# Optimization experiments

Hardware: AMD Instinct MI355X
Metric: run time of the kernel (lower is better)

## Reference

```python
import jax, jax.numpy as jnp
import numpy as np

CHUNK = 32


def l2norm(x):
    return x * jax.lax.rsqrt(jnp.sum(x * x, -1, keepdims=True) + 1e-6)


def causal_dwconv(x, w):
    # x: (b, l, C), w: (C, 1, k) -- depthwise causal 1D conv (left pad k-1)
    k = w.shape[-1]
    xt = jnp.transpose(x, (0, 2, 1))
    xt = jnp.pad(xt, ((0, 0), (0, 0), (k - 1, 0)))
    y = jax.lax.conv_general_dilated(xt, w, (1,), 'VALID',
                                     dimension_numbers=('NCH', 'OIH', 'NCH'),
                                     feature_group_count=xt.shape[1])
    return jnp.transpose(y, (0, 2, 1))


def delta_rule_chunkwise(q, k, v, beta):
    # q,k: (b,h,L,dk), v: (b,h,L,dv), beta: (b,h,L). L must be divisible by CHUNK.
    b, h, L, dk = q.shape
    dv = v.shape[-1]
    n = L // CHUNK
    q = l2norm(q)
    k = l2norm(k)
    v = v * beta[..., None]
    kb = k * beta[..., None]
    resh = lambda t: t.reshape(b, h, n, CHUNK, t.shape[-1])
    q, k, v, kb = (resh(t) for t in (q, k, v, kb))
    strict = jnp.tril(jnp.ones((CHUNK, CHUNK), bool), -1)
    A = jnp.where(strict, -(kb @ jnp.swapaxes(k, -1, -2)), 0.0)
    eye = jnp.eye(CHUNK, dtype=A.dtype)
    # UT transform: the sequential forward-substitution loop computes T = (I - A)^{-1}
    T = jax.scipy.linalg.solve_triangular(eye - A, jnp.broadcast_to(eye, A.shape), lower=True)
    u = T @ v
    w = T @ kb
    incl = jnp.tril(jnp.ones((CHUNK, CHUNK), bool))  # lower incl. diag

    def step(S, xs):
        q_i, k_i, u_i, w_i = xs
        attn = jnp.where(incl, q_i @ jnp.swapaxes(k_i, -1, -2), 0.0)
        u_hat = u_i - w_i @ S
        o_i = q_i @ S + attn @ u_hat
        return S + jnp.swapaxes(k_i, -1, -2) @ u_hat, o_i

    xs = tuple(jnp.moveaxis(t, 2, 0) for t in (q, k, u, w))
    S0 = jnp.zeros((b, h, dk, dv), q.dtype)
    S, o = jax.lax.scan(step, S0, xs)
    o = jnp.moveaxis(o, 0, 2).reshape(b, h, L, dv)
    return o, S


def branch_stats(x):
    # per-head stats over the feature dim: mean, std(ddof=1), mean|x|, L2 norm
    m = jnp.mean(x, -1, keepdims=True)
    s = jnp.std(x, -1, keepdims=True, ddof=1)
    a = jnp.mean(jnp.abs(x), -1, keepdims=True)
    l = jnp.sqrt(jnp.sum(x * x, -1, keepdims=True))
    return jnp.concatenate([m, s, a, l], -1)


def reference(hidden_states, q_w, k_w, v_w, b_w, qc_w, kc_w, vc_w,
              fir_w1, fir_w3, fir_w7, fir_w31,
              mlp_w1, mlp_b1, mlp_w2, mlp_b2, gate_log_temp, onorm_w, o_w):
    B, L, D = hidden_states.shape
    H = gate_log_temp.shape[0]
    dk = q_w.shape[1] // H
    dv = v_w.shape[1] // H
    # projections + causal short conv + silu
    q = jax.nn.silu(causal_dwconv(hidden_states @ q_w, qc_w))
    k = jax.nn.silu(causal_dwconv(hidden_states @ k_w, kc_w))
    v = jax.nn.silu(causal_dwconv(hidden_states @ v_w, vc_w))
    q = q.reshape(B, L, H, dk)
    k = k.reshape(B, L, H, dk)
    v_direct = v.reshape(B, L, H, dv)
    beta = jax.nn.sigmoid(hidden_states @ b_w)  # (B,L,H)
    delta_out, _ = delta_rule_chunkwise(
        jnp.transpose(q, (0, 2, 1, 3)), jnp.transpose(k, (0, 2, 1, 3)),
        jnp.transpose(v_direct, (0, 2, 1, 3)), jnp.transpose(beta, (0, 2, 1)))
    delta_out = jnp.transpose(delta_out, (0, 2, 1, 3))  # (B,L,H,dv)
    # multi-scale depthwise FIR branches on v
    v_flat = v_direct.reshape(B, L, H * dv)
    firs = [causal_dwconv(v_flat, w).reshape(B, L, H, dv)
            for w in (fir_w1, fir_w3, fir_w7, fir_w31)]
    branches = firs + [delta_out, v_direct]  # num_streams = 6
    S = len(branches)
    stats = jnp.concatenate([branch_stats(x) for x in branches], -1)  # (B,L,H,S*4)
    gate_in = jnp.concatenate([hidden_states, stats.reshape(B, L, H * S * 4)], -1)
    hgate = jax.nn.gelu(gate_in @ mlp_w1 + mlp_b1, approximate=False)
    logits = (hgate @ mlp_w2 + mlp_b2).reshape(B, L, H, S)
    temp = jax.nn.softplus(gate_log_temp) + 0.5  # min_gate_temp = 0.5
    weights = jax.nn.softmax(logits / temp[None, None, :, None], axis=-1)
    fused = sum(weights[..., i, None] * br for i, br in enumerate(branches))
    # RMSNorm over head_v_dim (eps=1e-5)
    fused = fused * jax.lax.rsqrt(jnp.mean(fused * fused, -1, keepdims=True) + 1e-5) * onorm_w
    return fused.reshape(B, L, H * dv) @ o_w


def setup_inputs() -> dict:
    key = jax.random.key(0)
    B, L, D, H = 2, 2048, 1024, 4
    dk = dv = D // H
    S = 6
    ks = iter(jax.random.split(key, 32))
    nrm = lambda shape, s=0.02: jax.random.normal(next(ks), shape, jnp.float32) * s

    def fir(kw):
        # delta init (last tap = 1) plus small noise
        base = jnp.zeros((H * dv, 1, kw), jnp.float32).at[:, 0, -1].set(1.0)
        return base + nrm((H * dv, 1, kw))

    gate_in_dim = D + S * 4 * H  # 1120
    hgd = D * 2 // 2             # 1024
    b2 = np.zeros(H * S, np.float32)
    for h in range(H):
        b2[h * S + S - 1] = 2.0  # value_bias_init on direct-value stream
    return {
        'hidden_states': jax.random.normal(next(ks), (B, L, D), jnp.float32),
        'q_w': nrm((D, D)), 'k_w': nrm((D, D)), 'v_w': nrm((D, D)),
        'b_w': nrm((D, H)),
        'qc_w': nrm((D, 1, 4), 0.3), 'kc_w': nrm((D, 1, 4), 0.3), 'vc_w': nrm((D, 1, 4), 0.3),
        'fir_w1': fir(1), 'fir_w3': fir(3), 'fir_w7': fir(7), 'fir_w31': fir(31),
        'mlp_w1': nrm((gate_in_dim, hgd)), 'mlp_b1': jnp.zeros((hgd,), jnp.float32),
        'mlp_w2': nrm((hgd, H * S)), 'mlp_b2': jnp.asarray(b2),
        'gate_log_temp': jnp.zeros((H,), jnp.float32),
        'onorm_w': jnp.ones((dv,), jnp.float32),
        'o_w': nrm((D, D)),
    }
```

## Files before the change

### kernel.cpp

```cpp
#include <hip/hip_runtime.h>
#include <hip/hip_bf16.h>
#include <math.h>

#define B_ 2
#define L_ 2048
#define D_ 1024
#define H_ 4
#define NC 64

typedef unsigned short ushort_t;
typedef __bf16 bf16x8 __attribute__((ext_vector_type(8)));
typedef float f32x4 __attribute__((ext_vector_type(4)));
typedef ushort_t u16x8 __attribute__((ext_vector_type(8)));
typedef short s16x8 __attribute__((ext_vector_type(8)));
typedef short s16x4 __attribute__((ext_vector_type(4)));

__device__ __forceinline__ ushort_t f2bs(float f) {
    __hip_bfloat16 h = __float2bfloat16(f);
    ushort_t u;
    __builtin_memcpy(&u, &h, 2);
    return u;
}

__device__ __forceinline__ float wred(float v) {
    v += __shfl_down(v, 32);
    v += __shfl_down(v, 16);
    v += __shfl_down(v, 8);
    v += __shfl_down(v, 4);
    v += __shfl_down(v, 2);
    v += __shfl_down(v, 1);
    return v;
}

__device__ __forceinline__ void gload16(const void* g, void* l) {
    __builtin_amdgcn_global_load_lds((const __attribute__((address_space(1))) void*)g,
                                     (__attribute__((address_space(3))) void*)l, 16, 0, 0);
}

__device__ __forceinline__ s16x4 pack4(float a, float b, float c, float d) {
    ushort4 u;
    u.x = f2bs(a); u.y = f2bs(b); u.z = f2bs(c); u.w = f2bs(d);
    return __builtin_bit_cast(s16x4, u);
}
__device__ __forceinline__ bf16x8 cat8(s16x4 lo, s16x4 hi) {
    s16x8 r = __builtin_shufflevector(lo, hi, 0, 1, 2, 3, 4, 5, 6, 7);
    return __builtin_bit_cast(bf16x8, r);
}

__global__ __launch_bounds__(256) void tcast_k(const float* __restrict__ W,
                                               ushort_t* __restrict__ WT, int K, int N) {
    __shared__ float tile[32 * 33];
    const int k0 = blockIdx.y << 5, n0 = blockIdx.x << 5;
    for (int e = threadIdx.x; e < 1024; e += 256)
        tile[(e >> 5) * 33 + (e & 31)] = W[(size_t)(k0 + (e >> 5)) * N + n0 + (e & 31)];
    __syncthreads();
    for (int e = threadIdx.x; e < 1024; e += 256)
        WT[(size_t)(n0 + (e >> 5)) * K + k0 + (e & 31)] = f2bs(tile[(e & 31) * 33 + (e >> 5)]);
}

__global__ __launch_bounds__(256) void cast_k(const float* __restrict__ x,
                                              ushort_t* __restrict__ y) {
    const int i = blockIdx.x * 256 + threadIdx.x;
    const float4 v = *(const float4*)&x[(size_t)i * 4];
    ushort4 p;
    p.x = f2bs(v.x); p.y = f2bs(v.y); p.z = f2bs(v.z); p.w = f2bs(v.w);
    *(ushort4*)&y[(size_t)i * 4] = p;
}

template <int ACT>
__global__ __launch_bounds__(256) void gemm_bf(const ushort_t* __restrict__ A,
                                               const ushort_t* __restrict__ Bt,
                                               const float* __restrict__ bias,
                                               float* __restrict__ C,
                                               int M, int N, int K) {
    __shared__ ushort_t As[128 * 32];
    __shared__ ushort_t Bs[128 * 32];
    const int t = threadIdx.x;
    const int wv = t >> 6, l = t & 63;
    const int m0 = blockIdx.y << 7, n0 = blockIdx.x << 7;
    const int wm = wv & 1, wn = wv >> 1;
    const int q4 = l >> 4, c16 = l & 15;
    f32x4 acc[4][4];
#pragma unroll
    for (int i = 0; i < 4; ++i)
#pragma unroll
        for (int j = 0; j < 4; ++j) {
            f32x4 z = {0.f, 0.f, 0.f, 0.f};
            acc[i][j] = z;
        }
    const int srow = (l >> 2);
    const int scol = (l & 3) << 3;
    for (int k0 = 0; k0 < K; k0 += 32) {
        __syncthreads();
#pragma unroll
        for (int si = 0; si < 2; ++si) {
            const int s = wv * 2 + si;
            gload16(&A[(size_t)(m0 + s * 16 + srow) * K + k0 + scol], &As[s * 512]);
            gload16(&Bt[(size_t)(n0 + s * 16 + srow) * K + k0 + scol], &Bs[s * 512]);
        }
        __syncthreads();
        bf16x8 af[4], bff[4];
#pragma unroll
        for (int mi = 0; mi < 4; ++mi)
            af[mi] = *(const bf16x8*)&As[(wm * 64 + mi * 16 + c16) * 32 + q4 * 8];
#pragma unroll
        for (int ni = 0; ni < 4; ++ni)
            bff[ni] = *(const bf16x8*)&Bs[(wn * 64 + ni * 16 + c16) * 32 + q4 * 8];
#pragma unroll
        for (int mi = 0; mi < 4; ++mi)
#pragma unroll
            for (int ni = 0; ni < 4; ++ni)
                acc[mi][ni] = __builtin_amdgcn_mfma_f32_16x16x32_bf16(af[mi], bff[ni],
                                                                     acc[mi][ni], 0, 0, 0);
    }
#pragma unroll
    for (int mi = 0; mi < 4; ++mi)
#pragma unroll
        for (int ni = 0; ni < 4; ++ni)
#pragma unroll
            for (int r = 0; r < 4; ++r) {
                const int row = m0 + wm * 64 + mi * 16 + q4 * 4 + r;
                const int col = n0 + wn * 64 + ni * 16 + c16;
                float v = acc[mi][ni][r];
                if (ACT == 1) {
                    v += bias[col];
                    v = 0.5f * v * (1.0f + erff(v * 0.70710678118654752f));
                }
                C[(size_t)row * N + col] = v;
            }
}

template <int DO_NORM, int EMIT_F32, int EMIT_BF>
__global__ __launch_bounds__(256) void convql_k(const float* __restrict__ X,
                                                const float* __restrict__ cw,
                                                float* __restrict__ Y,
                                                ushort_t* __restrict__ Ybf) {
    __shared__ float xs[35 * 256];
    const int bid = blockIdx.x;
    const int h = bid & 3, lt = (bid >> 2) & 63, b = bid >> 8;
    const int t = threadIdx.x;
    const int l0 = lt << 5;
    const int cg = (h << 8) | t;
    for (int e = t; e < 35 * 256; e += 256) {
        const int r = e >> 8, c = e & 255;
        const int gl = l0 + r - 3;
        xs[e] = (gl >= 0) ? X[((size_t)(b * L_) + gl) * 3072 + (h << 8) + c] : 0.f;
    }
    const float w0 = cw[cg * 4 + 0], w1 = cw[cg * 4 + 1];
    const float w2 = cw[cg * 4 + 2], w3 = cw[cg * 4 + 3];
    __syncthreads();
    float yr[32];
#pragma unroll
    for (int l = 0; l < 32; ++l) {
        const float a = xs[(l + 0) * 256 + t] * w0 + xs[(l + 1) * 256 + t] * w1 +
                        xs[(l + 2) * 256 + t] * w2 + xs[(l + 3) * 256 + t] * w3;
        yr[l] = a / (1.f + expf(-a));
    }
    if (DO_NORM) {
        __syncthreads();
#pragma unroll
        for (int l = 0; l < 32; ++l) xs[l * 256 + t] = yr[l];
        __syncthreads();
        const int wv = t >> 6, lane = t & 63;
#pragma unroll
        for (int ri = 0; ri < 8; ++ri) {
            const int r = wv * 8 + ri;
            float4 v = *(float4*)&xs[r * 256 + lane * 4];
            float ss = v.x * v.x + v.y * v.y + v.z * v.z + v.w * v.w;
            ss = wred(ss);
            ss = __shfl(ss, 0);
            const float s = rsqrtf(ss + 1e-6f);
            v.x *= s; v.y *= s; v.z *= s; v.w *= s;
            const size_t go = ((size_t)(b * L_) + l0 + r) * 1024 + (h << 8) + lane * 4;
            if (EMIT_F32) *(float4*)&Y[go] = v;
            if (EMIT_BF) {
                ushort4 p;
                p.x = f2bs(v.x); p.y = f2bs(v.y); p.z = f2bs(v.z); p.w = f2bs(v.w);
                *(ushort4*)&Ybf[go] = p;
            }
        }
    } else {
#pragma unroll
        for (int l = 0; l < 32; ++l)
            if (EMIT_F32) Y[((size_t)(b * L_) + l0 + l) * 1024 + cg] = yr[l];
    }
}

__global__ __launch_bounds__(256) void fir_k(const float* __restrict__ V,
                                             const float* __restrict__ w1w,
                                             const float* __restrict__ w3w,
                                             const float* __restrict__ w7w,
                                             const float* __restrict__ w31w,
                                             float* __restrict__ o1,
                                             float* __restrict__ o3,
                                             float* __restrict__ o7,
                                             float* __restrict__ o31) {
    __shared__ float xs[62 * 256];
    const int bid = blockIdx.x;
    const int h = bid & 3, lt = (bid >> 2) & 63, b = bid >> 8;
    const int t = threadIdx.x;
    const int l0 = lt << 5;
    const int cg = (h << 8) | t;
    for (int e = t; e < 62 * 256; e += 256) {
        const int r = e >> 8, c = e & 255;
        const int gl = l0 + r - 30;
        xs[e] = (gl >= 0) ? V[((size_t)(b * L_) + gl) * 1024 + (h << 8) + c] : 0.f;
    }
    float lw31[31], lw7[7], lw3[3];
#pragma unroll
    for (int j = 0; j < 31; ++j) lw31[j] = w31w[cg * 31 + j];
#pragma unroll
    for (int j = 0; j < 7; ++j) lw7[j] = w7w[cg * 7 + j];
#pragma unroll
    for (int j = 0; j < 3; ++j) lw3[j] = w3w[cg * 3 + j];
    const float lw1 = w1w[cg];
    __syncthreads();
    for (int l = 0; l < 32; ++l) {
        float a31 = 0.f, a7 = 0.f, a3 = 0.f, v = 0.f;
#pragma unroll
        for (int j = 0; j < 31; ++j) {
            v = xs[(l + j) * 256 + t];
            a31 += v * lw31[j];
            if (j >= 24) a7 += v * lw7[j - 24];
            if (j >= 28) a3 += v * lw3[j - 28];
        }
        const size_t go = ((size_t)(b * L_) + l0 + l) * 1024 + cg;
        o31[go] = a31;
        o7[go] = a7;
        o3[go] = a3;
        o1[go] = v * lw1;
    }
}

__global__ __launch_bounds__(64) void beta_k(const float* __restrict__ hs,
                                             const float* __restrict__ bw,
                                             float* __restrict__ beta,
                                             ushort_t* __restrict__ gin) {
    const int row = blockIdx.x;
    const int lane = threadIdx.x;
    float a0 = 0, a1 = 0, a2 = 0, a3 = 0;
    const float* hp = hs + (size_t)row * D_;
    ushort_t* gp = gin + (size_t)row * 1120;
    for (int c = lane; c < D_; c += 64) {
        const float x = hp[c];
        gp[c] = f2bs(x);
        a0 += x * bw[c * 4 + 0];
        a1 += x * bw[c * 4 + 1];
        a2 += x * bw[c * 4 + 2];
        a3 += x * bw[c * 4 + 3];
    }
    a0 = wred(a0); a1 = wred(a1); a2 = wred(a2); a3 = wred(a3);
    if (lane == 0) {
        float* o = beta + (size_t)row * 4;
        o[0] = 1.f / (1.f + expf(-a0));
        o[1] = 1.f / (1.f + expf(-a1));
        o[2] = 1.f / (1.f + expf(-a2));
        o[3] = 1.f / (1.f + expf(-a3));
    }
}

__global__ __launch_bounds__(256) void prep2_k(const ushort_t* __restrict__ qbf,
                                               const ushort_t* __restrict__ kbf,
                                               const float* __restrict__ vg,
                                               const float* __restrict__ beta,
                                               ushort_t* __restrict__ qfr,
                                               ushort_t* __restrict__ wfr,
                                               float* __restrict__ ufr,
                                               ushort_t* __restrict__ atfr,
                                               ushort_t* __restrict__ ktfr) {
    __shared__ ushort_t k_lds[32 * 264];
    __shared__ ushort_t kT_lds[256 * 32];
    __shared__ ushort_t vT_lds[256 * 32];
    __shared__ float Am[32 * 33];
    __shared__ float Tm[32 * 33];
    __shared__ ushort_t Tb[32 * 40];
    __shared__ ushort_t at_s[32 * 40];
    __shared__ float beta_s[32];
    const int bid = blockIdx.x;
    const int bh = bid >> 6, ci = bid & 63;
    const int b = bh >> 2, h = bh & 3;
    const int t = threadIdx.x;
    const int wv = t >> 6, lane = t & 63;
    const int mi = wv & 1, ni = wv >> 1;
    const int l16 = lane & 15, quad = lane >> 4;
    const size_t cb = (size_t)bid;
    const size_t grow = ((size_t)(b * L_ + ci * 32)) * 1024 + (h << 8);
    const f32x4 z4 = {0.f, 0.f, 0.f, 0.f};

    if (t < 32) beta_s[t] = beta[(size_t)(b * L_ + ci * 32 + t) * 4 + h];
#pragma unroll
    for (int j = 0; j < 4; ++j) {
        const int idx = j * 2048 + t * 8, r = idx >> 8, c = idx & 255;
        *(u16x8*)&k_lds[r * 264 + c] = *(const u16x8*)&kbf[grow + (size_t)r * 1024 + c];
    }
#pragma unroll
    for (int j = 0; j < 8; ++j) {
        const int e = j * 1024 + t * 4, r = e >> 8, c = e & 255;
        const float4 v4 = *(const float4*)&vg[grow + (size_t)r * 1024 + c];
        const float vv[4] = {v4.x, v4.y, v4.z, v4.w};
#pragma unroll
        for (int x = 0; x < 4; ++x) {
            const int cc = c + x;
            const int sp = (r >> 3) ^ ((cc >> 1) & 3);
            vT_lds[cc * 32 + sp * 8 + (r & 7)] = f2bs(vv[x]);
        }
    }
    f32x4 g = z4, atv = z4;
#pragma unroll
    for (int s = 0; s < 8; ++s) {
        const bf16x8 a =
            *(const bf16x8*)&kbf[grow + (size_t)(mi * 16 + l16) * 1024 + s * 32 + (quad << 3)];
        const bf16x8 bb =
            *(const bf16x8*)&kbf[grow + (size_t)(ni * 16 + l16) * 1024 + s * 32 + (quad << 3)];
        const bf16x8 qa =
            *(const bf16x8*)&qbf[grow + (size_t)(mi * 16 + l16) * 1024 + s * 32 + (quad << 3)];
        g = __builtin_amdgcn_mfma_f32_16x16x32_bf16(a, bb, g, 0, 0, 0);
        atv = __builtin_amdgcn_mfma_f32_16x16x32_bf16(qa, bb, atv, 0, 0, 0);
        if (ni == 0) {
            const size_t ga = grow + (size_t)(mi * 16 + l16) * 1024 + s * 32 + (quad << 2);
            const ushort4 q0 = *(const ushort4*)&qbf[ga];
            const ushort4 q1 = *(const ushort4*)&qbf[ga + 16];
            ushort_t* qd = &qfr[((cb * 2 + mi) * 8 + s) * 512 + lane * 8];
            *(ushort4*)qd = q0;
            *(ushort4*)(qd + 4) = q1;
        }
    }
    __syncthreads();
#pragma unroll
    for (int r = 0; r < 4; ++r) {
        const int row = mi * 16 + (quad << 2) + r;
        const int col = ni * 16 + l16;
        Am[row * 33 + col] = (col < row) ? -beta_s[row] * g[r] : 0.f;
        Tm[row * 33 + col] = (row == col) ? 1.f : 0.f;
        at_s[row * 40 + col] = (col <= row) ? f2bs(atv[r]) : (ushort_t)0;
    }
#pragma unroll
    for (int j = 0; j < 8; ++j) {
        const int e = j * 1024 + t * 4, r = e >> 8, c = e & 255;
#pragma unroll
        for (int x = 0; x < 4; ++x) {
            const int cc = c + x;
            const int sp = (r >> 3) ^ ((cc >> 1) & 3);
            kT_lds[cc * 32 + sp * 8 + (r & 7)] = k_lds[r * 264 + cc];
        }
    }
    __syncthreads();
    if (wv < 2) {
        const int ra = (wv * 16 + l16) * 40 + (quad << 2);
        const ushort4 a0 = *(const ushort4*)&at_s[ra];
        const ushort4 a1 = *(const ushort4*)&at_s[ra + 16];
        ushort_t* ad = &atfr[(cb * 2 + wv) * 512 + lane * 8];
        *(ushort4*)ad = a0;
        *(ushort4*)(ad + 4) = a1;
    }
#pragma unroll
    for (int j2 = 0; j2 < 4; ++j2) {
        const int tc = wv * 4 + j2;
        const int d = tc * 16 + l16;
        const int x = (d >> 1) & 3;
        const int base = d * 32 + ((quad & 1) << 2);
        const ushort4 k0 = *(const ushort4*)&kT_lds[base + ((((quad >> 1) + 0) ^ x) << 3)];
        const ushort4 k1 = *(const ushort4*)&kT_lds[base + ((((quad >> 1) + 2) ^ x) << 3)];
        ushort_t* kd = &ktfr[(cb * 16 + tc) * 512 + lane * 8];
        *(ushort4*)kd = k0;
        *(ushort4*)(kd + 4) = k1;
    }
    for (int i = 1; i < 32; ++i) {
        if (t < 32) {
            float s = 0.f;
            for (int j = 0; j < i; ++j) s += Am[i * 33 + j] * Tm[j * 33 + t];
            Tm[i * 33 + t] += s;
        }
        __syncthreads();
    }
#pragma unroll
    for (int j = 0; j < 4; ++j) {
        const int e = j * 256 + t, i = e >> 5, jj = e & 31;
        Tb[i * 40 + jj] = f2bs(Tm[i * 33 + jj] * beta_s[jj]);
    }
    __syncthreads();
    const bf16x8 tf = *(const bf16x8*)&Tb[(mi * 16 + l16) * 40 + (quad << 3)];
#pragma unroll
    for (int j = 0; j < 8; ++j) {
        const int nt = ni * 8 + j;
        const int d = (nt << 4) + l16;
        const int sp = quad ^ ((d >> 1) & 3);
        const bf16x8 kb = *(const bf16x8*)&kT_lds[d * 32 + (sp << 3)];
        const bf16x8 vb = *(const bf16x8*)&vT_lds[d * 32 + (sp << 3)];
        const f32x4 wacc = __builtin_amdgcn_mfma_f32_16x16x32_bf16(tf, kb, z4, 0, 0, 0);
        const f32x4 uacc = __builtin_amdgcn_mfma_f32_16x16x32_bf16(tf, vb, z4, 0, 0, 0);
        *(float4*)&ufr[((cb * 16 + nt) * 2 + mi) * 256 + lane * 4] =
            make_float4(uacc[0], uacc[1], uacc[2], uacc[3]);
#pragma unroll
        for (int r = 0; r < 4; ++r) {
            const int row = mi * 16 + (quad << 2) + r;
            k_lds[row * 264 + d] = f2bs(wacc[r]);
        }
    }
    __syncthreads();
    if (wv < 2) {
#pragma unroll
        for (int sp = 0; sp < 8; ++sp) {
            const int rb = (wv * 16 + l16) * 264 + sp * 32 + (quad << 2);
            const ushort4 w0 = *(const ushort4*)&k_lds[rb];
            const ushort4 w1 = *(const ushort4*)&k_lds[rb + 16];
            ushort_t* wd = &wfr[((cb * 2 + wv) * 8 + sp) * 512 + lane * 8];
            *(ushort4*)wd = w0;
            *(ushort4*)(wd + 4) = w1;
        }
    }
}

__global__ __launch_bounds__(64, 1) void scan9_k(const ushort_t* __restrict__ qfr,
                                                 const ushort_t* __restrict__ wfr,
                                                 const float* __restrict__ ufr,
                                                 const ushort_t* __restrict__ atfr,
                                                 const ushort_t* __restrict__ ktfr,
                                                 float* __restrict__ dlt) {
    __shared__ ushort_t qstg[2][16 * 512];
    __shared__ ushort_t wstg[2][16 * 512];
    __shared__ ushort_t atstg[2][2 * 512];
    __shared__ float ustg[2][2 * 256];
    const int l = threadIdx.x;
    const int qd = l >> 4, c = l & 15;
    const int bh = blockIdx.x & 7, tile = blockIdx.x >> 3;
    const int b = bh >> 2, h = bh & 3;

    f32x4 Sacc[16];
    s16x4 SB[16];
#pragma unroll
    for (int tc = 0; tc < 16; ++tc) {
        f32x4 z = {0.f, 0.f, 0.f, 0.f};
        Sacc[tc] = z;
        s16x4 zs = {0, 0, 0, 0};
        SB[tc] = zs;
    }
    s16x8 ktA[16], ktB[16];

    auto stage = [&](int ci, int p) {
        const size_t cb = (size_t)(bh * NC + ci);
        const ushort_t* qsrc = qfr + cb * (16 * 512);
        const ushort_t* wsrc = wfr + cb * (16 * 512);
#pragma unroll
        for (int f = 0; f < 16; ++f) gload16(&qsrc[f * 512 + l * 8], &qstg[p][f * 512]);
#pragma unroll
        for (int f = 0; f < 16; ++f) gload16(&wsrc[f * 512 + l * 8], &wstg[p][f * 512]);
#pragma unroll
        for (int hf = 0; hf < 2; ++hf)
            gload16(&atfr[(cb * 2 + hf) * 512 + l * 8], &atstg[p][hf * 512]);
#pragma unroll
        for (int hf = 0; hf < 2; ++hf)
            gload16(&ufr[((cb * 16 + tile) * 2 + hf) * 256 + l * 4], &ustg[p][hf * 256]);
    };

    {
        const ushort_t* ksrc = ktfr + (size_t)(bh * NC) * (16 * 512);
#pragma unroll
        for (int tc = 0; tc < 16; ++tc) ktA[tc] = *(const s16x8*)&ksrc[tc * 512 + l * 8];
    }
    stage(0, 0);
    asm volatile("s_waitcnt vmcnt(0)" ::: "memory");
    __builtin_amdgcn_sched_barrier(0);

#define SC_BODY(CI, P, KT, KTN)                                                              \
    {                                                                                        \
        asm volatile("s_waitcnt vmcnt(8)" ::: "memory");                                     \
        __builtin_amdgcn_sched_barrier(0);                                                   \
        if ((CI) + 1 < NC) {                                                                 \
            const ushort_t* ksrc = ktfr + (size_t)(bh * NC + (CI) + 1) * (16 * 512);         \
            _Pragma("unroll") for (int tc = 0; tc < 16; ++tc)                                \
                KTN[tc] = *(const s16x8*)&ksrc[tc * 512 + l * 8];                            \
            stage((CI) + 1, (P) ^ 1);                                                        \
        }                                                                                    \
        f32x4 aw[2], oq[2];                                                                  \
        _Pragma("unroll") for (int hf = 0; hf < 2; ++hf) {                                   \
            f32x4 z = {0.f, 0.f, 0.f, 0.f};                                                  \
            aw[hf] = z;                                                                      \
            oq[hf] = z;                                                                      \
        }                                                                                    \
        _Pragma("unroll") for (int sp = 0; sp < 8; ++sp) {                                   \
            const bf16x8 Sop = cat8(SB[2 * sp + 0], SB[2 * sp + 1]);                         \
            _Pragma("unroll") for (int hf = 0; hf < 2; ++hf) {                               \
                const bf16x8 wv8 = *(const bf16x8*)&wstg[P][(hf * 8 + sp) * 512 + l * 8];    \
                const bf16x8 qv8 = *(const bf16x8*)&qstg[P][(hf * 8 + sp) * 512 + l * 8];    \
                aw[hf] = __builtin_amdgcn_mfma_f32_16x16x32_bf16(wv8, Sop, aw[hf], 0, 0, 0); \
                oq[hf] = __builtin_amdgcn_mfma_f32_16x16x32_bf16(qv8, Sop, oq[hf], 0, 0, 0); \
            }                                                                                \
        }                                                                                    \
        s16x4 uhB[2];                                                                        \
        _Pragma("unroll") for (int hf = 0; hf < 2; ++hf) {                                   \
            const float4 uv = *(const float4*)&ustg[P][hf * 256 + l * 4];                    \
            uhB[hf] = pack4(uv.x - aw[hf][0], uv.y - aw[hf][1],                              \
                            uv.z - aw[hf][2], uv.w - aw[hf][3]);                             \
        }                                                                                    \
        const bf16x8 Uop = cat8(uhB[0], uhB[1]);                                             \
        _Pragma("unroll") for (int tc = 0; tc < 16; ++tc) {                                  \
            Sacc[tc] = __builtin_amdgcn_mfma_f32_16x16x32_bf16(                              \
                __builtin_bit_cast(bf16x8, KT[tc]), Uop, Sacc[tc], 0, 0, 0);                 \
            SB[tc] = pack4(Sacc[tc][0], Sacc[tc][1], Sacc[tc][2], Sacc[tc][3]);              \
        }                                                                                    \
        _Pragma("unroll") for (int hf = 0; hf < 2; ++hf) {                                   \
            const bf16x8 av = *(const bf16x8*)&atstg[P][hf * 512 + l * 8];                   \
            oq[hf] = __builtin_amdgcn_mfma_f32_16x16x32_bf16(av, Uop, oq[hf], 0, 0, 0);      \
        }                                                                                    \
        const size_t gbase =                                                                 \
            ((size_t)(b * L_ + (CI) * 32)) * 1024 + (h << 8) + (tile << 4) + c;              \
        _Pragma("unroll") for (int hf = 0; hf < 2; ++hf)                                     \
            _Pragma("unroll") for (int r = 0; r < 4; ++r)                                    \
                dlt[gbase + (size_t)(hf * 16 + (qd << 2) + r) * 1024] = oq[hf][r];           \
    }

    for (int ci = 0; ci < NC; ci += 2) {
        SC_BODY(ci, 0, ktA, ktB)
        SC_BODY(ci + 1, 1, ktB, ktA)
    }
#undef SC_BODY
}

__global__ __launch_bounds__(64) void stats_k(const float* __restrict__ f1,
                                              const float* __restrict__ f3,
                                              const float* __restrict__ f7,
                                              const float* __restrict__ f31,
                                              const float* __restrict__ dl,
                                              const float* __restrict__ vv,
                                              ushort_t* __restrict__ gin) {
    const int row = blockIdx.x;
    const int lane = threadIdx.x;
    const float* ptrs[6] = {f1, f3, f7, f31, dl, vv};
    const size_t base = (size_t)row * 256;
    ushort_t* gp = gin + (size_t)(row >> 2) * 1120 + 1024 + (row & 3) * 24;
    for (int br = 0; br < 6; ++br) {
        const float4 x = *(const float4*)&ptrs[br][base + lane * 4];
        float s1 = x.x + x.y + x.z + x.w;
        float s2 = x.x * x.x + x.y * x.y + x.z * x.z + x.w * x.w;
        float sa = fabsf(x.x) + fabsf(x.y) + fabsf(x.z) + fabsf(x.w);
        s1 = wred(s1); s2 = wred(s2); sa = wred(sa);
        if (lane == 0) {
            const float m = s1 / 256.f;
            float var = (s2 - 256.f * m * m) / 255.f;
            if (var < 0.f) var = 0.f;
            gp[br * 4 + 0] = f2bs(m);
            gp[br * 4 + 1] = f2bs(sqrtf(var));
            gp[br * 4 + 2] = f2bs(sa / 256.f);
            gp[br * 4 + 3] = f2bs(sqrtf(s2));
        }
    }
}

__global__ __launch_bounds__(256) void wts_k(const float* __restrict__ hg,
                                             const float* __restrict__ w2,
                                             const float* __restrict__ b2,
                                             const float* __restrict__ glt,
                                             float* __restrict__ wts) {
    const int row = blockIdx.x;
    const int h = threadIdx.x >> 6, lane = threadIdx.x & 63;
    float hv[16];
    const float* hp = hg + (size_t)row * 1024;
#pragma unroll
    for (int ii = 0; ii < 16; ++ii) hv[ii] = hp[lane + 64 * ii];
    float lg[6];
#pragma unroll
    for (int s = 0; s < 6; ++s) {
        const int j = h * 6 + s;
        float acc = 0.f;
#pragma unroll
        for (int ii = 0; ii < 16; ++ii) acc += hv[ii] * w2[(size_t)(lane + 64 * ii) * 24 + j];
        lg[s] = wred(acc);
    }
    if (lane == 0) {
        const float temp = log1pf(expf(glt[h])) + 0.5f;
        float mx = -1e30f;
#pragma unroll
        for (int s = 0; s < 6; ++s) {
            lg[s] = (lg[s] + b2[h * 6 + s]) / temp;
            mx = fmaxf(mx, lg[s]);
        }
        float se = 0.f;
#pragma unroll
        for (int s = 0; s < 6; ++s) {
            lg[s] = expf(lg[s] - mx);
            se += lg[s];
        }
        float* o = &wts[(size_t)row * 24 + h * 6];
        const float inv = 1.f / se;
#pragma unroll
        for (int s = 0; s < 6; ++s) o[s] = lg[s] * inv;
    }
}

__global__ __launch_bounds__(1024) void fuse_k(const float* __restrict__ f1,
                                               const float* __restrict__ f3,
                                               const float* __restrict__ f7,
                                               const float* __restrict__ f31,
                                               const float* __restrict__ dl,
                                               const float* __restrict__ vv,
                                               const float* __restrict__ wts,
                                               const float* __restrict__ onw,
                                               ushort_t* __restrict__ fused) {
    __shared__ float wloc[24];
    __shared__ float psum[16];
    const int row = blockIdx.x, t = threadIdx.x;
    if (t < 24) wloc[t] = wts[(size_t)row * 24 + t];
    __syncthreads();
    const int h = t >> 8, dd = t & 255;
    const size_t idx = (size_t)row * 1024 + t;
    const float* ptrs[6] = {f1, f3, f7, f31, dl, vv};
    float f = 0.f;
#pragma unroll
    for (int br = 0; br < 6; ++br) f += wloc[h * 6 + br] * ptrs[br][idx];
    float ss = wred(f * f);
    const int wave = t >> 6;
    if ((t & 63) == 0) psum[wave] = ss;
    __syncthreads();
    const float tot = psum[h * 4 + 0] + psum[h * 4 + 1] + psum[h * 4 + 2] + psum[h * 4 + 3];
    const float scale = rsqrtf(tot / 256.f + 1e-5f);
    fused[idx] = f2bs(f * scale * onw[dd]);
}

extern "C" void kernel_launch(void* const* d_in, const int* in_sizes, int n_in,
                              void* d_out, int out_size, void* d_ws, size_t ws_size,
                              hipStream_t stream) {
    const float* hs   = (const float*)d_in[0];
    const float* q_w  = (const float*)d_in[1];
    const float* k_w  = (const float*)d_in[2];
    const float* v_w  = (const float*)d_in[3];
    const float* b_w  = (const float*)d_in[4];
    const float* qc_w = (const float*)d_in[5];
    const float* kc_w = (const float*)d_in[6];
    const float* vc_w = (const float*)d_in[7];
    const float* f1w  = (const float*)d_in[8];
    const float* f3w  = (const float*)d_in[9];
    const float* f7w  = (const float*)d_in[10];
    const float* f31w = (const float*)d_in[11];
    const float* w1   = (const float*)d_in[12];
    const float* b1   = (const float*)d_in[13];
    const float* w2   = (const float*)d_in[14];
    const float* b2   = (const float*)d_in[15];
    const float* glt  = (const float*)d_in[16];
    const float* onw  = (const float*)d_in[17];
    const float* o_w  = (const float*)d_in[18];
    float* out = (float*)d_out;

    const size_t SZ = (size_t)B_ * L_ * D_;
    float* qlin = (float*)d_ws;
    float* klin = qlin + SZ;
    float* vlin = klin + SZ;
    float* qbuf = vlin + SZ;
    float* kbuf = qbuf + SZ;
    float* vbuf = kbuf + SZ;
    float* f31b = vbuf + SZ;
    float* wb   = f31b + SZ;
    float* ub   = wb + SZ;
    float* dlt  = ub + SZ;
    float* beta = dlt + SZ;
    float* attn = beta + (size_t)B_ * L_ * H_;
    float* f1b = qlin;
    float* f3b = klin;
    float* f7b = vlin;
    float* hgate = kbuf;
    float* qkv = qlin;
    float* wts = attn + (size_t)B_ * H_ * NC * 1024;

    ushort_t* hs_bf = (ushort_t*)dlt;
    ushort_t* qwT = (ushort_t*)f31b;
    ushort_t* kwT = (ushort_t*)f31b + 1048576;
    ushort_t* vwT = (ushort_t*)f31b + 2097152;
    ushort_t* qbf = (ushort_t*)f31b + 3145728;
    ushort_t* kbf = (ushort_t*)kbuf;
    ushort_t* gin_bf = (ushort_t*)qbuf;
    ushort_t* w1T = (ushort_t*)(wb + 2359296);
    ushort_t* owT = (ushort_t*)ub;
    ushort_t* fused_bf = (ushort_t*)kbuf;
    ushort_t* ktfr = (ushort_t*)klin;
    ushort_t* qfr = (ushort_t*)klin + SZ;
    ushort_t* wfr = (ushort_t*)wb;
    float* ufr = ub;
    ushort_t* atfr = (ushort_t*)attn;

    const int M = B_ * L_;

    tcast_k<<<dim3(32, 32), 256, 0, stream>>>(q_w, qwT, 1024, 1024);
    tcast_k<<<dim3(32, 32), 256, 0, stream>>>(k_w, kwT, 1024, 1024);
    tcast_k<<<dim3(32, 32), 256, 0, stream>>>(v_w, vwT, 1024, 1024);
    cast_k<<<4096, 256, 0, stream>>>(hs, hs_bf);
    gemm_bf<0><<<dim3(24, 32), 256, 0, stream>>>(hs_bf, qwT, nullptr, qkv, M, 3072, 1024);
    beta_k<<<M, 64, 0, stream>>>(hs, b_w, beta, gin_bf);
    convql_k<1, 0, 1><<<512, 256, 0, stream>>>(qkv + 0,    qc_w, nullptr, qbf);
    convql_k<1, 0, 1><<<512, 256, 0, stream>>>(qkv + 1024, kc_w, nullptr, kbf);
    convql_k<0, 1, 0><<<512, 256, 0, stream>>>(qkv + 2048, vc_w, vbuf, nullptr);
    prep2_k<<<B_ * H_ * NC, 256, 0, stream>>>(qbf, kbf, vbuf, beta, qfr, wfr, ufr, atfr, ktfr);
    scan9_k<<<128, 64, 0, stream>>>(qfr, wfr, ufr, atfr, ktfr, dlt);
    fir_k<<<512, 256, 0, stream>>>(vbuf, f1w, f3w, f7w, f31w, f1b, f3b, f7b, f31b);
    stats_k<<<M * H_, 64, 0, stream>>>(f1b, f3b, f7b, f31b, dlt, vbuf, gin_bf);
    tcast_k<<<dim3(32, 35), 256, 0, stream>>>(w1, w1T, 1120, 1024);
    gemm_bf<1><<<dim3(8, 32), 256, 0, stream>>>(gin_bf, w1T, b1, hgate, M, 1024, 1120);
    wts_k<<<M, 256, 0, stream>>>(hgate, w2, b2, glt, wts);
    fuse_k<<<M, 1024, 0, stream>>>(f1b, f3b, f7b, f31b, dlt, vbuf, wts, onw, fused_bf);
    tcast_k<<<dim3(32, 32), 256, 0, stream>>>(o_w, owT, 1024, 1024);
    gemm_bf<0><<<dim3(8, 32), 256, 0, stream>>>(fused_bf, owT, nullptr, out, M, 1024, 1024);
}
```

Before: 564.9 us.

## Process two value tiles per scan block, sharing staged q/w/kt chunks

The chunked delta-rule scan kernel now assigns two 16-wide value tiles to each single-wave block, so the grid shrinks from 128 to 64 blocks. The q, w and kᵀ fragments for each chunk are staged once and reused by both tiles' MFMAs, which halves global traffic for these operands. Running two independent state chains in one wave gives the MFMA pipeline more independent work per step. kᵀ is now double-buffered through LDS with async loads instead of being held in registers. The trade-off is fewer concurrent blocks on the device, roughly double the accumulator registers per wave, and a larger LDS footprint.

```diff
diff --git a/kernel.cpp b/kernel.cpp
--- a/kernel.cpp
+++ b/kernel.cpp
@@ -411,110 +411,136 @@
     }
 }
 
-__global__ __launch_bounds__(64, 1) void scan9_k(const ushort_t* __restrict__ qfr,
-                                                 const ushort_t* __restrict__ wfr,
-                                                 const float* __restrict__ ufr,
-                                                 const ushort_t* __restrict__ atfr,
-                                                 const ushort_t* __restrict__ ktfr,
-                                                 float* __restrict__ dlt) {
+__global__ __launch_bounds__(64, 1) void scan10_k(const ushort_t* __restrict__ qfr,
+                                                  const ushort_t* __restrict__ wfr,
+                                                  const float* __restrict__ ufr,
+                                                  const ushort_t* __restrict__ atfr,
+                                                  const ushort_t* __restrict__ ktfr,
+                                                  float* __restrict__ dlt) {
     __shared__ ushort_t qstg[2][16 * 512];
     __shared__ ushort_t wstg[2][16 * 512];
+    __shared__ ushort_t ktstg[2][16 * 512];
     __shared__ ushort_t atstg[2][2 * 512];
-    __shared__ float ustg[2][2 * 256];
+    __shared__ float ustg[2][4 * 256];
     const int l = threadIdx.x;
     const int qd = l >> 4, c = l & 15;
-    const int bh = blockIdx.x & 7, tile = blockIdx.x >> 3;
+    const int bh = blockIdx.x & 7, pair = blockIdx.x >> 3;
+    const int t0 = pair * 2;
     const int b = bh >> 2, h = bh & 3;
 
-    f32x4 Sacc[16];
-    s16x4 SB[16];
-#pragma unroll
-    for (int tc = 0; tc < 16; ++tc) {
-        f32x4 z = {0.f, 0.f, 0.f, 0.f};
-        Sacc[tc] = z;
-        s16x4 zs = {0, 0, 0, 0};
-        SB[tc] = zs;
-    }
-    s16x8 ktA[16], ktB[16];
+    f32x4 Sacc[2][16];
+    s16x4 SB[2][16];
+#pragma unroll
+    for (int tt = 0; tt < 2; ++tt)
+#pragma unroll
+        for (int tc = 0; tc < 16; ++tc) {
+            f32x4 z = {0.f, 0.f, 0.f, 0.f};
+            Sacc[tt][tc] = z;
+            s16x4 zs = {0, 0, 0, 0};
+            SB[tt][tc] = zs;
+        }
 
     auto stage = [&](int ci, int p) {
         const size_t cb = (size_t)(bh * NC + ci);
         const ushort_t* qsrc = qfr + cb * (16 * 512);
         const ushort_t* wsrc = wfr + cb * (16 * 512);
+        const ushort_t* ksrc = ktfr + cb * (16 * 512);
 #pragma unroll
         for (int f = 0; f < 16; ++f) gload16(&qsrc[f * 512 + l * 8], &qstg[p][f * 512]);
 #pragma unroll
         for (int f = 0; f < 16; ++f) gload16(&wsrc[f * 512 + l * 8], &wstg[p][f * 512]);
+#pragma unroll
+        for (int f = 0; f < 16; ++f) gload16(&ksrc[f * 512 + l * 8], &ktstg[p][f * 512]);
 #pragma unroll
         for (int hf = 0; hf < 2; ++hf)
             gload16(&atfr[(cb * 2 + hf) * 512 + l * 8], &atstg[p][hf * 512]);
 #pragma unroll
-        for (int hf = 0; hf < 2; ++hf)
-            gload16(&ufr[((cb * 16 + tile) * 2 + hf) * 256 + l * 4], &ustg[p][hf * 256]);
+        for (int tt = 0; tt < 2; ++tt)
+#pragma unroll
+            for (int hf = 0; hf < 2; ++hf)
+                gload16(&ufr[((cb * 16 + t0 + tt) * 2 + hf) * 256 + l * 4],
+                        &ustg[p][(tt * 2 + hf) * 256]);
     };
 
-    {
-        const ushort_t* ksrc = ktfr + (size_t)(bh * NC) * (16 * 512);
-#pragma unroll
-        for (int tc = 0; tc < 16; ++tc) ktA[tc] = *(const s16x8*)&ksrc[tc * 512 + l * 8];
-    }
     stage(0, 0);
     asm volatile("s_waitcnt vmcnt(0)" ::: "memory");
     __builtin_amdgcn_sched_barrier(0);
 
-#define SC_BODY(CI, P, KT, KTN)                                                              \
-    {                                                                                        \
-        asm volatile("s_waitcnt vmcnt(8)" ::: "memory");                                     \
-        __builtin_amdgcn_sched_barrier(0);                                                   \
-        if ((CI) + 1 < NC) {                                                                 \
-            const ushort_t* ksrc = ktfr + (size_t)(bh * NC + (CI) + 1) * (16 * 512);         \
-            _Pragma("unroll") for (int tc = 0; tc < 16; ++tc)                                \
-                KTN[tc] = *(const s16x8*)&ksrc[tc * 512 + l * 8];                            \
-            stage((CI) + 1, (P) ^ 1);                                                        \
-        }                                                                                    \
-        f32x4 aw[2], oq[2];                                                                  \
-        _Pragma("unroll") for (int hf = 0; hf < 2; ++hf) {                                   \
-            f32x4 z = {0.f, 0.f, 0.f, 0.f};                                                  \
-            aw[hf] = z;                                                                      \
-            oq[hf] = z;                                                                      \
-        }                                                                                    \
-        _Pragma("unroll") for (int sp = 0; sp < 8; ++sp) {                                   \
-            const bf16x8 Sop = cat8(SB[2 * sp + 0], SB[2 * sp + 1]);                         \
-            _Pragma("unroll") for (int hf = 0; hf < 2; ++hf) {                               \
-                const bf16x8 wv8 = *(const bf16x8*)&wstg[P][(hf * 8 + sp) * 512 + l * 8];    \
-                const bf16x8 qv8 = *(const bf16x8*)&qstg[P][(hf * 8 + sp) * 512 + l * 8];    \
-                aw[hf] = __builtin_amdgcn_mfma_f32_16x16x32_bf16(wv8, Sop, aw[hf], 0, 0, 0); \
-                oq[hf] = __builtin_amdgcn_mfma_f32_16x16x32_bf16(qv8, Sop, oq[hf], 0, 0, 0); \
-            }                                                                                \
-        }                                                                                    \
-        s16x4 uhB[2];                                                                        \
-        _Pragma("unroll") for (int hf = 0; hf < 2; ++hf) {                                   \
-            const float4 uv = *(const float4*)&ustg[P][hf * 256 + l * 4];                    \
-            uhB[hf] = pack4(uv.x - aw[hf][0], uv.y - aw[hf][1],                              \
-                            uv.z - aw[hf][2], uv.w - aw[hf][3]);                             \
-        }                                                                                    \
-        const bf16x8 Uop = cat8(uhB[0], uhB[1]);                                             \
-        _Pragma("unroll") for (int tc = 0; tc < 16; ++tc) {                                  \
-            Sacc[tc] = __builtin_amdgcn_mfma_f32_16x16x32_bf16(                              \
-                __builtin_bit_cast(bf16x8, KT[tc]), Uop, Sacc[tc], 0, 0, 0);                 \
-            SB[tc] = pack4(Sacc[tc][0], Sacc[tc][1], Sacc[tc][2], Sacc[tc][3]);              \
-        }                                                                                    \
-        _Pragma("unroll") for (int hf = 0; hf < 2; ++hf) {                                   \
-            const bf16x8 av = *(const bf16x8*)&atstg[P][hf * 512 + l * 8];                   \
-            oq[hf] = __builtin_amdgcn_mfma_f32_16x16x32_bf16(av, Uop, oq[hf], 0, 0, 0);      \
-        }                                                                                    \
-        const size_t gbase =                                                                 \
-            ((size_t)(b * L_ + (CI) * 32)) * 1024 + (h << 8) + (tile << 4) + c;              \
-        _Pragma("unroll") for (int hf = 0; hf < 2; ++hf)                                     \
-            _Pragma("unroll") for (int r = 0; r < 4; ++r)                                    \
-                dlt[gbase + (size_t)(hf * 16 + (qd << 2) + r) * 1024] = oq[hf][r];           \
-    }
-
-    for (int ci = 0; ci < NC; ci += 2) {
-        SC_BODY(ci, 0, ktA, ktB)
-        SC_BODY(ci + 1, 1, ktB, ktA)
-    }
-#undef SC_BODY
+    for (int ci = 0; ci < NC; ++ci) {
+        const int p = ci & 1;
+        asm volatile("s_waitcnt vmcnt(8)" ::: "memory");
+        __builtin_amdgcn_sched_barrier(0);
+        if (ci + 1 < NC) stage(ci + 1, p ^ 1);
+
+        f32x4 aw[2][2], oq[2][2];
+#pragma unroll
+        for (int tt = 0; tt < 2; ++tt)
+#pragma unroll
+            for (int hf = 0; hf < 2; ++hf) {
+                f32x4 z = {0.f, 0.f, 0.f, 0.f};
+                aw[tt][hf] = z;
+                oq[tt][hf] = z;
+            }
+#pragma unroll
+        for (int sp = 0; sp < 8; ++sp) {
+            bf16x8 Sop[2];
+#pragma unroll
+            for (int tt = 0; tt < 2; ++tt)
+                Sop[tt] = cat8(SB[tt][2 * sp + 0], SB[tt][2 * sp + 1]);
+#pragma unroll
+            for (int hf = 0; hf < 2; ++hf) {
+                const bf16x8 wv8 = *(const bf16x8*)&wstg[p][(hf * 8 + sp) * 512 + l * 8];
+                const bf16x8 qv8 = *(const bf16x8*)&qstg[p][(hf * 8 + sp) * 512 + l * 8];
+#pragma unroll
+                for (int tt = 0; tt < 2; ++tt) {
+                    aw[tt][hf] =
+                        __builtin_amdgcn_mfma_f32_16x16x32_bf16(wv8, Sop[tt], aw[tt][hf], 0, 0, 0);
+                    oq[tt][hf] =
+                        __builtin_amdgcn_mfma_f32_16x16x32_bf16(qv8, Sop[tt], oq[tt][hf], 0, 0, 0);
+                }
+            }
+        }
+        bf16x8 Uop[2];
+#pragma unroll
+        for (int tt = 0; tt < 2; ++tt) {
+            s16x4 uhB[2];
+#pragma unroll
+            for (int hf = 0; hf < 2; ++hf) {
+                const float4 uv = *(const float4*)&ustg[p][(tt * 2 + hf) * 256 + l * 4];
+                uhB[hf] = pack4(uv.x - aw[tt][hf][0], uv.y - aw[tt][hf][1],
+                                uv.z - aw[tt][hf][2], uv.w - aw[tt][hf][3]);
+            }
+            Uop[tt] = cat8(uhB[0], uhB[1]);
+        }
+#pragma unroll
+        for (int tc = 0; tc < 16; ++tc) {
+            const bf16x8 ktv = *(const bf16x8*)&ktstg[p][tc * 512 + l * 8];
+#pragma unroll
+            for (int tt = 0; tt < 2; ++tt) {
+                Sacc[tt][tc] = __builtin_amdgcn_mfma_f32_16x16x32_bf16(ktv, Uop[tt],
+                                                                       Sacc[tt][tc], 0, 0, 0);
+                SB[tt][tc] = pack4(Sacc[tt][tc][0], Sacc[tt][tc][1], Sacc[tt][tc][2],
+                                   Sacc[tt][tc][3]);
+            }
+        }
+#pragma unroll
+        for (int hf = 0; hf < 2; ++hf) {
+            const bf16x8 av = *(const bf16x8*)&atstg[p][hf * 512 + l * 8];
+#pragma unroll
+            for (int tt = 0; tt < 2; ++tt)
+                oq[tt][hf] =
+                    __builtin_amdgcn_mfma_f32_16x16x32_bf16(av, Uop[tt], oq[tt][hf], 0, 0, 0);
+        }
+        const size_t gb0 = ((size_t)(b * L_ + ci * 32)) * 1024 + (h << 8) + c;
+#pragma unroll
+        for (int tt = 0; tt < 2; ++tt)
+#pragma unroll
+            for (int hf = 0; hf < 2; ++hf)
+#pragma unroll
+                for (int r = 0; r < 4; ++r)
+                    dlt[gb0 + ((t0 + tt) << 4) + (size_t)(hf * 16 + (qd << 2) + r) * 1024] =
+                        oq[tt][hf][r];
+    }
 }
 
 __global__ __launch_bounds__(64) void stats_k(const float* __restrict__ f1,
@@ -689,7 +715,7 @@
     convql_k<1, 0, 1><<<512, 256, 0, stream>>>(qkv + 1024, kc_w, nullptr, kbf);
     convql_k<0, 1, 0><<<512, 256, 0, stream>>>(qkv + 2048, vc_w, vbuf, nullptr);
     prep2_k<<<B_ * H_ * NC, 256, 0, stream>>>(qbf, kbf, vbuf, beta, qfr, wfr, ufr, atfr, ktfr);
-    scan9_k<<<128, 64, 0, stream>>>(qfr, wfr, ufr, atfr, ktfr, dlt);
+    scan10_k<<<64, 64, 0, stream>>>(qfr, wfr, ufr, atfr, ktfr, dlt);
     fir_k<<<512, 256, 0, stream>>>(vbuf, f1w, f3w, f7w, f31w, f1b, f3b, f7b, f31b);
     stats_k<<<M * H_, 64, 0, stream>>>(f1b, f3b, f7b, f31b, dlt, vbuf, gin_bf);
     tcast_k<<<dim3(32, 35), 256, 0, stream>>>(w1, w1T, 1120, 1024);
```

Measured after the change: 649.9 us. 1.15x slower.
